# Optimization experiments

Measured on AMD Instinct MI355X. Metric: run time of the kernel, lower is better.

Reference implementation:

```python
import jax, jax.numpy as jnp
import numpy as np

B, T, V, D, P, DEP = 64, 32, 32000, 1024, 8, 4
TAU = 1.0
EPS = 1e-5


def setup_inputs() -> dict:
    key = jax.random.key(0)
    ks = jax.random.split(key, 9)
    s = 0.02
    x = jax.random.randint(ks[0], (B, T), 0, V)
    emb = jax.random.normal(ks[1], (V, D), jnp.float32) * s
    pos = jax.random.normal(ks[2], (T, D), jnp.float32) * s
    # primitive library: n_prims MLPs (Linear -> GELU -> Linear), stacked
    w1 = jax.random.normal(ks[3], (P, D, D), jnp.float32) * s
    b1 = jnp.zeros((P, D), jnp.float32)
    w2 = jax.random.normal(ks[4], (P, D, D), jnp.float32) * s
    b2 = jnp.zeros((P, D), jnp.float32)
    # one selector Linear(dim, n_prims) per depth
    sel_w = jax.random.normal(ks[5], (DEP, P, D), jnp.float32) * s
    sel_b = jnp.zeros((DEP, P), jnp.float32)
    ln_g = jnp.ones((D,), jnp.float32)
    ln_b = jnp.zeros((D,), jnp.float32)
    head_w = jax.random.normal(ks[6], (V, D), jnp.float32) * s
    # fixed gumbel noise (replaces torch's in-op sampling, kept deterministic)
    u = jax.random.uniform(ks[7], (DEP, B, P), jnp.float32, 1e-6, 1.0 - 1e-6)
    gumbel = -jnp.log(-jnp.log(u))
    return dict(x=x, emb=emb, pos=pos, w1=w1, b1=b1, w2=w2, b2=b2,
                sel_w=sel_w, sel_b=sel_b, ln_g=ln_g, ln_b=ln_b,
                head_w=head_w, gumbel=gumbel)


def reference(x, emb, pos, w1, b1, w2, b2, sel_w, sel_b, ln_g, ln_b, head_w, gumbel):
    h = emb[x] + pos[None, :x.shape[1], :]          # [B,T,D]
    div = jnp.float32(0.0)
    unif = jnp.float32(1.0 / P)
    for d in range(DEP):
        ctx = h.mean(axis=1)                         # [B,D]
        logits = ctx @ sel_w[d].T + sel_b[d]         # [B,P]
        weights = jax.nn.softmax((logits + gumbel[d]) / TAU, axis=-1)
        # all primitives over all tokens at once (grouped GEMM), no T loop
        u1 = jax.nn.gelu(jnp.einsum('btd,pde->btpe', h, w1) + b1, approximate=False)
        prim = jnp.einsum('btpe,pef->btpf', u1, w2) + b2   # [B,T,P,D]
        h = h + jnp.einsum('btpf,bp->btf', prim, weights)  # residual add
        avg = weights.mean(axis=0)                   # [P]
        # F.kl_div(avg.log(), uniform, reduction='sum')
        div = div + jnp.sum(unif * (jnp.log(unif) - jnp.log(avg)))
    mu = h.mean(-1, keepdims=True)
    var = ((h - mu) ** 2).mean(-1, keepdims=True)
    hn = (h - mu) * jax.lax.rsqrt(var + EPS) * ln_g + ln_b
    return hn @ head_w.T, div
```

## Files before the change

kernel.cpp:

```cpp
#include <hip/hip_runtime.h>
#include <hip/hip_bf16.h>
#include <math.h>

typedef __bf16 bf16x8 __attribute__((ext_vector_type(8)));
typedef float  f32x4  __attribute__((ext_vector_type(4)));

struct __align__(8) bf16x4s { __hip_bfloat16 a, b, c, d; };

__device__ __forceinline__ void gload_lds16(const void* g, void* l) {
  __builtin_amdgcn_global_load_lds(
      (const __attribute__((address_space(1))) void*)g,
      (__attribute__((address_space(3))) void*)l, 16, 0, 0);
}

__device__ __forceinline__ float fast_gelu(float v) {
  float s = 0.70710678118654752f * v;
  float a = fabsf(s);
  float t = __builtin_amdgcn_rcpf(fmaf(0.3275911f, a, 1.0f));
  float p = t * fmaf(t, fmaf(t, fmaf(t, fmaf(t, 1.061405429f, -1.453152027f),
                                     1.421413741f), -0.284496736f), 0.254829592f);
  float e = __expf(-a * a);
  float er = copysignf(fmaf(-p, e, 1.0f), s);
  return 0.5f * v * (1.0f + er);
}

#define BAR()   asm volatile("s_barrier" ::: "memory")
#define LGKM0() do { asm volatile("s_waitcnt lgkmcnt(0)" ::: "memory"); \
                     __builtin_amdgcn_sched_barrier(0); } while (0)
#define VMC(N)  do { asm volatile("s_waitcnt vmcnt(" #N ")" ::: "memory"); \
                     __builtin_amdgcn_sched_barrier(0); } while (0)
#define P1()    __builtin_amdgcn_s_setprio(1)
#define P0()    __builtin_amdgcn_s_setprio(0)

template<int EPI>
__global__ __launch_bounds__(512, 2)
void gemm_nt(const __hip_bfloat16* __restrict__ A,
             const __hip_bfloat16* __restrict__ B,
             const int K, const int Kc, const int N,
             const float* __restrict__ p0,
             const float* __restrict__ p1,
             float* __restrict__ f32out,
             __hip_bfloat16* __restrict__ bfout)
{
  __shared__ __align__(16) __hip_bfloat16 lds[65536];

  const int tid = threadIdx.x;
  const int lane = tid & 63, wid = tid >> 6;
  const int l15 = lane & 15, l4 = lane >> 4;
  const int r8 = lane >> 3, blk = lane & 7;
  const int wm = wid >> 2, wn = wid & 3;

  const int nx = gridDim.x;
  const int flat = blockIdx.x + nx * blockIdx.y;
  const int q = (nx * gridDim.y) >> 3;
  const int nid = (flat & 7) * q + (flat >> 3);
  const long m0 = (long)(nid % nx) * 256;
  const long n0 = (long)(nid / nx) * 256;

  const int kbeg = blockIdx.z * Kc;
  const int nt = Kc / 64;

  f32x4 acc[8][4] = {};
  bf16x8 ar[4][2], br[4][2];

  auto stageA = [&](int buf, int h, int k0) {
#pragma unroll
    for (int p2 = 0; p2 < 2; ++p2) {
      int ch = p2 * 16 + h * 8 + wid;
      int row = ch * 8 + r8;
      gload_lds16(A + (m0 + row) * (long)K + k0 + ((blk ^ r8) << 3),
                  lds + buf * 16384 + ch * 512);
    }
  };
  auto stageB = [&](int buf, int h, int k0) {
#pragma unroll
    for (int p2 = 0; p2 < 2; ++p2) {
      int ch = (p2 * 2 + (wid >> 2)) * 8 + h * 4 + (wid & 3);
      int row = ch * 8 + r8;
      gload_lds16(B + (n0 + row) * (long)K + k0 + ((blk ^ r8) << 3),
                  lds + 32768 + buf * 16384 + ch * 512);
    }
  };
  auto readA = [&](const __hip_bfloat16* pA, int mih) {
#pragma unroll
    for (int mi = 0; mi < 4; ++mi)
#pragma unroll
      for (int kk = 0; kk < 2; ++kk) {
        int row = wm * 128 + mih * 64 + mi * 16 + l15;
        ar[mi][kk] = *(const bf16x8*)(pA + row * 64 + (((kk * 4 + l4) ^ (row & 7)) << 3));
      }
  };
  auto readB2 = [&](const __hip_bfloat16* pB, int njh) {
#pragma unroll
    for (int nj = 0; nj < 2; ++nj)
#pragma unroll
      for (int kk = 0; kk < 2; ++kk) {
        int row = wn * 64 + njh * 32 + nj * 16 + l15;
        br[njh * 2 + nj][kk] = *(const bf16x8*)(pB + row * 64 + (((kk * 4 + l4) ^ (row & 7)) << 3));
      }
  };
  auto mfma8 = [&](int mib, int njb) {
#pragma unroll
    for (int mi = 0; mi < 4; ++mi)
#pragma unroll
      for (int nj = 0; nj < 2; ++nj)
#pragma unroll
        for (int kk = 0; kk < 2; ++kk)
          acc[mib + mi][njb + nj] = __builtin_amdgcn_mfma_f32_16x16x32_bf16(
              ar[mi][kk], br[njb + nj][kk], acc[mib + mi][njb + nj], 0, 0, 0);
  };

  stageA(0, 0, kbeg);
  stageB(0, 0, kbeg);
  stageB(0, 1, kbeg);
  stageA(0, 1, kbeg);
  stageA(1, 0, kbeg + 64);
  stageB(1, 0, kbeg + 64);
  stageB(1, 1, kbeg + 64);
  VMC(10);
  BAR();

  for (int s = 0; s < nt - 2; ++s) {
    const int b = s & 1;
    const __hip_bfloat16* pA = lds + b * 16384;
    const __hip_bfloat16* pB = lds + 32768 + b * 16384;
    const int k1 = kbeg + (s + 1) * 64, k2 = kbeg + (s + 2) * 64;
    readA(pA, 0); readB2(pB, 0);
    stageA(b ^ 1, 1, k1);
    BAR(); LGKM0();
    P1(); mfma8(0, 0); P0();
    VMC(10); BAR();
    readB2(pB, 1);
    stageA(b, 0, k2);
    BAR(); LGKM0();
    P1(); mfma8(0, 2); P0();
    VMC(10); BAR();
    readA(pA, 1);
    stageB(b, 0, k2);
    BAR(); LGKM0();
    P1(); mfma8(4, 0); P0();
    BAR();
    stageB(b, 1, k2);
    BAR();
    P1(); mfma8(4, 2); P0();
    VMC(10); BAR();
  }

  {
    const int b = (nt - 2) & 1;
    const __hip_bfloat16* pA = lds + b * 16384;
    const __hip_bfloat16* pB = lds + 32768 + b * 16384;
    readA(pA, 0); readB2(pB, 0);
    stageA(b ^ 1, 1, kbeg + (nt - 1) * 64);
    BAR(); LGKM0();
    P1(); mfma8(0, 0); P0();
    VMC(10); BAR();
    readB2(pB, 1);
    BAR(); LGKM0();
    P1(); mfma8(0, 2); P0();
    VMC(8); BAR();
    readA(pA, 1);
    BAR(); LGKM0();
    P1(); mfma8(4, 0); P0();
    BAR();
    BAR();
    P1(); mfma8(4, 2); P0();
    VMC(4); BAR();
  }
  {
    const int b = (nt - 1) & 1;
    const __hip_bfloat16* pA = lds + b * 16384;
    const __hip_bfloat16* pB = lds + 32768 + b * 16384;
    readA(pA, 0); readB2(pB, 0);
    BAR(); LGKM0();
    P1(); mfma8(0, 0); P0();
    VMC(2); BAR();
    readB2(pB, 1);
    BAR(); LGKM0();
    P1(); mfma8(0, 2); P0();
    VMC(0); BAR();
    readA(pA, 1);
    BAR(); LGKM0();
    P1(); mfma8(4, 0); P0();
    BAR();
    BAR();
    P1(); mfma8(4, 2); P0();
    BAR();
  }

  const long slab = (EPI == 2) ? (long)blockIdx.z * (long)(gridDim.x * 256) * N : 0;
#pragma unroll
  for (int mi = 0; mi < 8; ++mi) {
    const long gmb = m0 + wm * 128 + mi * 16 + l4 * 4;
    const int b = (int)(gmb >> 5);
#pragma unroll
    for (int nj = 0; nj < 4; ++nj) {
      const long gn = n0 + wn * 64 + nj * 16 + l15;
      if constexpr (EPI == 0) {
        const int p = (int)(gn >> 10), e = (int)(gn & 1023);
        const float bias = p0[(p << 10) + e];
        const float wpb = p1[(b << 3) + p];
#pragma unroll
        for (int r = 0; r < 4; ++r) {
          float v = fast_gelu(acc[mi][nj][r] + bias) * wpb;
          bfout[(gmb + r) * (long)N + gn] = __float2bfloat16(v);
        }
      } else {
#pragma unroll
        for (int r = 0; r < 4; ++r)
          f32out[slab + (gmb + r) * (long)N + gn] = acc[mi][nj][r];
      }
    }
  }
}

__global__ void cvt_bf16_k(const float* __restrict__ in, __hip_bfloat16* __restrict__ out, long n) {
  long i = ((long)blockIdx.x * blockDim.x + threadIdx.x) * 4;
  if (i >= n) return;
  float4 v = *(const float4*)(in + i);
  *(bf16x4s*)(out + i) = bf16x4s{__float2bfloat16(v.x), __float2bfloat16(v.y),
                                 __float2bfloat16(v.z), __float2bfloat16(v.w)};
}

__global__ void tconv_k(const float* __restrict__ in, __hip_bfloat16* __restrict__ out,
                        long in_bs, long out_rs, long out_bs) {
  __shared__ float tile[32][33];
  int p = blockIdx.z;
  int r0 = blockIdx.y * 32, c0 = blockIdx.x * 32;
  int tx = threadIdx.x, ty = threadIdx.y;
#pragma unroll
  for (int i = 0; i < 32; i += 8)
    tile[ty + i][tx] = in[(long)p * in_bs + (long)(r0 + ty + i) * 1024 + c0 + tx];
  __syncthreads();
#pragma unroll
  for (int i = 0; i < 32; i += 8)
    out[(long)(c0 + ty + i) * out_rs + (long)p * out_bs + (r0 + tx)] =
        __float2bfloat16(tile[tx][ty + i]);
}

__global__ void embed_k(const int* __restrict__ x, const float* __restrict__ emb,
                        const float* __restrict__ pos, float* __restrict__ h,
                        __hip_bfloat16* __restrict__ hb, float* __restrict__ divp) {
  int row = blockIdx.x;
  int t = row & 31;
  int c = threadIdx.x * 4;
  long tok = x[row];
  float4 e = *(const float4*)(emb + tok * 1024 + c);
  float4 q = *(const float4*)(pos + (long)t * 1024 + c);
  float4 v{e.x + q.x, e.y + q.y, e.z + q.z, e.w + q.w};
  *(float4*)(h + (long)row * 1024 + c) = v;
  *(bf16x4s*)(hb + (long)row * 1024 + c) =
      bf16x4s{__float2bfloat16(v.x), __float2bfloat16(v.y),
              __float2bfloat16(v.z), __float2bfloat16(v.w)};
  if (row == 0 && threadIdx.x == 0) *divp = 0.f;
}

__global__ void select_k(const float* __restrict__ h, const float* __restrict__ selw,
                         const float* __restrict__ selb, const float* __restrict__ gum,
                         float* __restrict__ W, int dep) {
  int b = blockIdx.x, tid = threadIdx.x;
  int c = tid * 4;
  float4 s{0.f, 0.f, 0.f, 0.f};
  for (int t = 0; t < 32; ++t) {
    const float4 v = *(const float4*)(h + ((long)(b * 32 + t)) * 1024 + c);
    s.x += v.x; s.y += v.y; s.z += v.z; s.w += v.w;
  }
  float lp[8];
#pragma unroll
  for (int p = 0; p < 8; ++p) {
    const float4 w = *(const float4*)(selw + dep * 8192 + p * 1024 + c);
    lp[p] = (s.x * w.x + s.y * w.y + s.z * w.z + s.w * w.w) * (1.f / 32.f);
  }
  int lane = tid & 63, wid = tid >> 6;
#pragma unroll
  for (int p = 0; p < 8; ++p)
    for (int o = 32; o; o >>= 1) lp[p] += __shfl_down(lp[p], o);
  __shared__ float red[4][8];
  if (lane == 0) {
#pragma unroll
    for (int p = 0; p < 8; ++p) red[wid][p] = lp[p];
  }
  __syncthreads();
  if (tid == 0) {
    float lg[8], mx = -1e30f;
    for (int p = 0; p < 8; ++p) {
      lg[p] = red[0][p] + red[1][p] + red[2][p] + red[3][p]
            + selb[dep * 8 + p] + gum[dep * 512 + b * 8 + p];
      mx = fmaxf(mx, lg[p]);
    }
    float sm = 0.f;
    for (int p = 0; p < 8; ++p) { lg[p] = expf(lg[p] - mx); sm += lg[p]; }
    float inv = 1.f / sm;
    for (int p = 0; p < 8; ++p) W[b * 8 + p] = lg[p] * inv;
  }
}

__global__ void wb2_k(const float* __restrict__ W, const float* __restrict__ b2,
                      float* __restrict__ wb2, float* __restrict__ divp) {
  int b = blockIdx.x;
  int c = threadIdx.x * 4;
  float4 a{0.f, 0.f, 0.f, 0.f};
#pragma unroll
  for (int p = 0; p < 8; ++p) {
    float wp = W[b * 8 + p];
    const float4 v = *(const float4*)(b2 + p * 1024 + c);
    a.x += wp * v.x; a.y += wp * v.y; a.z += wp * v.z; a.w += wp * v.w;
  }
  *(float4*)(wb2 + (long)b * 1024 + c) = a;
  if (b == 0 && threadIdx.x == 0) {
    float s[8] = {0.f, 0.f, 0.f, 0.f, 0.f, 0.f, 0.f, 0.f};
    for (int bb = 0; bb < 64; ++bb)
#pragma unroll
      for (int p = 0; p < 8; ++p) s[p] += W[bb * 8 + p];
    float d = *divp;
    const float u = 0.125f, lu = logf(0.125f);
#pragma unroll
    for (int p = 0; p < 8; ++p) d += u * (lu - logf(s[p] * (1.f / 64.f)));
    *divp = d;
  }
}

__global__ void h_update_k(const float* __restrict__ part, float* __restrict__ h,
                           const float* __restrict__ wb2, __hip_bfloat16* __restrict__ hb) {
  int row = blockIdx.x;
  int c = threadIdx.x * 4;
  long idx = (long)row * 1024 + c;
  float4 a = *(const float4*)(h + idx);
  const float4 w = *(const float4*)(wb2 + (long)(row >> 5) * 1024 + c);
  a.x += w.x; a.y += w.y; a.z += w.z; a.w += w.w;
#pragma unroll
  for (int s = 0; s < 8; ++s) {
    const float4 v = *(const float4*)(part + (long)s * 2097152 + idx);
    a.x += v.x; a.y += v.y; a.z += v.z; a.w += v.w;
  }
  *(float4*)(h + idx) = a;
  *(bf16x4s*)(hb + idx) = bf16x4s{__float2bfloat16(a.x), __float2bfloat16(a.y),
                                  __float2bfloat16(a.z), __float2bfloat16(a.w)};
}

__global__ void ln_k(const float* __restrict__ h, const float* __restrict__ g,
                     const float* __restrict__ be, __hip_bfloat16* __restrict__ hnb,
                     const float* __restrict__ divp, float* __restrict__ divout) {
  int row = blockIdx.x, tid = threadIdx.x;
  int c = tid * 4;
  const float4 v = *(const float4*)(h + (long)row * 1024 + c);
  float s = v.x + v.y + v.z + v.w;
  float q = v.x * v.x + v.y * v.y + v.z * v.z + v.w * v.w;
  for (int o = 32; o; o >>= 1) { s += __shfl_down(s, o); q += __shfl_down(q, o); }
  __shared__ float red[16];
  int lane = tid & 63, wid = tid >> 6;
  if (lane == 0) { red[wid] = s; red[8 + wid] = q; }
  __syncthreads();
  if (tid == 0) {
    float S = red[0] + red[1] + red[2] + red[3];
    float Q = red[8] + red[9] + red[10] + red[11];
    float mu = S * (1.f / 1024.f);
    float var = Q * (1.f / 1024.f) - mu * mu;
    red[0] = mu; red[1] = rsqrtf(var + 1e-5f);
  }
  __syncthreads();
  float mu = red[0], rs = red[1];
  float4 gg = *(const float4*)(g + c), bb = *(const float4*)(be + c);
  *(bf16x4s*)(hnb + (long)row * 1024 + c) =
      bf16x4s{__float2bfloat16((v.x - mu) * rs * gg.x + bb.x),
              __float2bfloat16((v.y - mu) * rs * gg.y + bb.y),
              __float2bfloat16((v.z - mu) * rs * gg.z + bb.z),
              __float2bfloat16((v.w - mu) * rs * gg.w + bb.w)};
  if (row == 0 && tid == 0) *divout = *divp;
}

extern "C" void kernel_launch(void* const* d_in, const int* in_sizes, int n_in,
                              void* d_out, int out_size, void* d_ws, size_t ws_size,
                              hipStream_t stream) {
  (void)in_sizes; (void)n_in; (void)out_size; (void)ws_size;
  const int*   x     = (const int*)  d_in[0];
  const float* emb   = (const float*)d_in[1];
  const float* pos   = (const float*)d_in[2];
  const float* w1    = (const float*)d_in[3];
  const float* b1    = (const float*)d_in[4];
  const float* w2    = (const float*)d_in[5];
  const float* b2    = (const float*)d_in[6];
  const float* selw  = (const float*)d_in[7];
  const float* selb  = (const float*)d_in[8];
  const float* lng   = (const float*)d_in[9];
  const float* lnb   = (const float*)d_in[10];
  const float* headw = (const float*)d_in[11];
  const float* gum   = (const float*)d_in[12];
  float* out = (float*)d_out;

  char* ws = (char*)d_ws;
  __hip_bfloat16* w1t   = (__hip_bfloat16*)(ws);
  __hip_bfloat16* w2t   = (__hip_bfloat16*)(ws + 16777216);
  __hip_bfloat16* headb = (__hip_bfloat16*)(ws + 33554432);
  float*          h     = (float*)(ws + 99090432);
  __hip_bfloat16* hb    = (__hip_bfloat16*)(ws + 107479040);
  __hip_bfloat16* u1    = (__hip_bfloat16*)(ws + 111673344);
  float*          W     = (float*)(ws + 145227776);
  float*          wb2   = (float*)(ws + 145229824);
  float*          divp  = (float*)(ws + 145491968);
  float*          part  = out;

  cvt_bf16_k<<<32000, 256, 0, stream>>>(headw, headb, 32768000L);
  tconv_k<<<dim3(32, 32, 8), dim3(32, 8), 0, stream>>>(w1, w1t, 1L << 20, 1024L, 1L << 20);
  tconv_k<<<dim3(32, 32, 8), dim3(32, 8), 0, stream>>>(w2, w2t, 1L << 20, 8192L, 1024L);
  embed_k<<<2048, 256, 0, stream>>>(x, emb, pos, h, hb, divp);

  for (int d = 0; d < 4; ++d) {
    select_k<<<64, 256, 0, stream>>>(h, selw, selb, gum, W, d);
    wb2_k<<<64, 256, 0, stream>>>(W, b2, wb2, divp);
    gemm_nt<0><<<dim3(8, 32), 512, 0, stream>>>(hb, w1t, 1024, 1024, 8192, b1, W, nullptr, u1);
    gemm_nt<2><<<dim3(8, 4, 8), 512, 0, stream>>>(u1, w2t, 8192, 1024, 1024, nullptr, nullptr, part, nullptr);
    h_update_k<<<2048, 256, 0, stream>>>(part, h, wb2, hb);
  }

  ln_k<<<2048, 256, 0, stream>>>(h, lng, lnb, hb, divp, out + 65536000L);
  gemm_nt<2><<<dim3(8, 125), 512, 0, stream>>>(hb, headb, 1024, 1024, 32000, nullptr, nullptr, out, nullptr);
}
```

Before: 655.8 us.

## Double-buffer GEMM fragment registers and fuse selector with bias-weighting kernel

The GEMM main loop now holds separate early and late register sets for the A and B fragments. It prefetches the next stage's fragments while the MFMAs run on the current ones, which removes the lgkmcnt(0) waits and several barriers per quarter-step. The selector and weighted-bias kernels are merged into one launch, the KL-divergence reduction moves into h_update, and per-depth weights are kept in separate slices. The head GEMM output uses nontemporal stores. The new overlap needs more VGPRs, which could hurt occupancy or cause spills, and the relaxed waits depend on the compiler placing LDS wait counts correctly.

```diff
diff --git a/kernel.cpp b/kernel.cpp
--- a/kernel.cpp
+++ b/kernel.cpp
@@ -25,12 +25,23 @@
 }
 
 #define BAR()   asm volatile("s_barrier" ::: "memory")
-#define LGKM0() do { asm volatile("s_waitcnt lgkmcnt(0)" ::: "memory"); \
-                     __builtin_amdgcn_sched_barrier(0); } while (0)
+#define SB0()   __builtin_amdgcn_sched_barrier(0)
 #define VMC(N)  do { asm volatile("s_waitcnt vmcnt(" #N ")" ::: "memory"); \
                      __builtin_amdgcn_sched_barrier(0); } while (0)
 #define P1()    __builtin_amdgcn_s_setprio(1)
 #define P0()    __builtin_amdgcn_s_setprio(0)
+
+#define MQ(MB, NB, AV, BV)                                                    \
+  do {                                                                        \
+    _Pragma("unroll")                                                         \
+    for (int mi_ = 0; mi_ < 4; ++mi_)                                         \
+      _Pragma("unroll")                                                       \
+      for (int nj_ = 0; nj_ < 2; ++nj_)                                       \
+        _Pragma("unroll")                                                     \
+        for (int kk_ = 0; kk_ < 2; ++kk_)                                     \
+          acc[MB + mi_][NB + nj_] = __builtin_amdgcn_mfma_f32_16x16x32_bf16(  \
+              AV[mi_][kk_], BV[nj_][kk_], acc[MB + mi_][NB + nj_], 0, 0, 0);  \
+  } while (0)
 
 template<int EPI>
 __global__ __launch_bounds__(512, 2)
@@ -61,7 +72,7 @@
   const int nt = Kc / 64;
 
   f32x4 acc[8][4] = {};
-  bf16x8 ar[4][2], br[4][2];
+  bf16x8 arE[4][2], arL[4][2], brE[2][2], brL[2][2];
 
   auto stageA = [&](int buf, int h, int k0) {
 #pragma unroll
@@ -81,33 +92,45 @@
                   lds + 32768 + buf * 16384 + ch * 512);
     }
   };
-  auto readA = [&](const __hip_bfloat16* pA, int mih) {
+  auto readAE = [&](int buf) {
+    const __hip_bfloat16* pA = lds + buf * 16384;
 #pragma unroll
     for (int mi = 0; mi < 4; ++mi)
 #pragma unroll
       for (int kk = 0; kk < 2; ++kk) {
-        int row = wm * 128 + mih * 64 + mi * 16 + l15;
-        ar[mi][kk] = *(const bf16x8*)(pA + row * 64 + (((kk * 4 + l4) ^ (row & 7)) << 3));
+        int row = wm * 128 + mi * 16 + l15;
+        arE[mi][kk] = *(const bf16x8*)(pA + row * 64 + (((kk * 4 + l4) ^ (row & 7)) << 3));
       }
   };
-  auto readB2 = [&](const __hip_bfloat16* pB, int njh) {
+  auto readAL = [&](int buf) {
+    const __hip_bfloat16* pA = lds + buf * 16384;
+#pragma unroll
+    for (int mi = 0; mi < 4; ++mi)
+#pragma unroll
+      for (int kk = 0; kk < 2; ++kk) {
+        int row = wm * 128 + 64 + mi * 16 + l15;
+        arL[mi][kk] = *(const bf16x8*)(pA + row * 64 + (((kk * 4 + l4) ^ (row & 7)) << 3));
+      }
+  };
+  auto readBE = [&](int buf) {
+    const __hip_bfloat16* pB = lds + 32768 + buf * 16384;
 #pragma unroll
     for (int nj = 0; nj < 2; ++nj)
 #pragma unroll
       for (int kk = 0; kk < 2; ++kk) {
-        int row = wn * 64 + njh * 32 + nj * 16 + l15;
-        br[njh * 2 + nj][kk] = *(const bf16x8*)(pB + row * 64 + (((kk * 4 + l4) ^ (row & 7)) << 3));
+        int row = wn * 64 + nj * 16 + l15;
+        brE[nj][kk] = *(const bf16x8*)(pB + row * 64 + (((kk * 4 + l4) ^ (row & 7)) << 3));
       }
   };
-  auto mfma8 = [&](int mib, int njb) {
-#pragma unroll
-    for (int mi = 0; mi < 4; ++mi)
-#pragma unroll
-      for (int nj = 0; nj < 2; ++nj)
-#pragma unroll
-        for (int kk = 0; kk < 2; ++kk)
-          acc[mib + mi][njb + nj] = __builtin_amdgcn_mfma_f32_16x16x32_bf16(
-              ar[mi][kk], br[njb + nj][kk], acc[mib + mi][njb + nj], 0, 0, 0);
+  auto readBL = [&](int buf) {
+    const __hip_bfloat16* pB = lds + 32768 + buf * 16384;
+#pragma unroll
+    for (int nj = 0; nj < 2; ++nj)
+#pragma unroll
+      for (int kk = 0; kk < 2; ++kk) {
+        int row = wn * 64 + 32 + nj * 16 + l15;
+        brL[nj][kk] = *(const bf16x8*)(pB + row * 64 + (((kk * 4 + l4) ^ (row & 7)) << 3));
+      }
   };
 
   stageA(0, 0, kbeg);
@@ -117,75 +140,66 @@
   stageA(1, 0, kbeg + 64);
   stageB(1, 0, kbeg + 64);
   stageB(1, 1, kbeg + 64);
-  VMC(10);
+  VMC(8);
   BAR();
+  readAE(0); readBE(0);
 
   for (int s = 0; s < nt - 2; ++s) {
     const int b = s & 1;
-    const __hip_bfloat16* pA = lds + b * 16384;
-    const __hip_bfloat16* pB = lds + 32768 + b * 16384;
     const int k1 = kbeg + (s + 1) * 64, k2 = kbeg + (s + 2) * 64;
-    readA(pA, 0); readB2(pB, 0);
+    readBL(b);
     stageA(b ^ 1, 1, k1);
-    BAR(); LGKM0();
-    P1(); mfma8(0, 0); P0();
-    VMC(10); BAR();
-    readB2(pB, 1);
+    SB0();
+    P1(); MQ(0, 0, arE, brE); P0();
+    VMC(8); BAR();
+    readAL(b);
     stageA(b, 0, k2);
-    BAR(); LGKM0();
-    P1(); mfma8(0, 2); P0();
-    VMC(10); BAR();
-    readA(pA, 1);
+    SB0();
+    P1(); MQ(0, 2, arE, brL); P0();
+    VMC(8); BAR();
+    readAE(b ^ 1);
     stageB(b, 0, k2);
-    BAR(); LGKM0();
-    P1(); mfma8(4, 0); P0();
-    BAR();
+    SB0();
+    P1(); MQ(4, 0, arL, brE); P0();
+    VMC(8); BAR();
+    readBE(b ^ 1);
     stageB(b, 1, k2);
-    BAR();
-    P1(); mfma8(4, 2); P0();
-    VMC(10); BAR();
+    SB0();
+    P1(); MQ(4, 2, arL, brL); P0();
+    VMC(8); BAR();
   }
 
   {
     const int b = (nt - 2) & 1;
-    const __hip_bfloat16* pA = lds + b * 16384;
-    const __hip_bfloat16* pB = lds + 32768 + b * 16384;
-    readA(pA, 0); readB2(pB, 0);
+    readBL(b);
     stageA(b ^ 1, 1, kbeg + (nt - 1) * 64);
-    BAR(); LGKM0();
-    P1(); mfma8(0, 0); P0();
-    VMC(10); BAR();
-    readB2(pB, 1);
-    BAR(); LGKM0();
-    P1(); mfma8(0, 2); P0();
+    SB0();
+    P1(); MQ(0, 0, arE, brE); P0();
     VMC(8); BAR();
-    readA(pA, 1);
-    BAR(); LGKM0();
-    P1(); mfma8(4, 0); P0();
-    BAR();
-    BAR();
-    P1(); mfma8(4, 2); P0();
+    readAL(b);
+    SB0();
+    P1(); MQ(0, 2, arE, brL); P0();
+    VMC(6); BAR();
+    readAE(b ^ 1);
+    SB0();
+    P1(); MQ(4, 0, arL, brE); P0();
     VMC(4); BAR();
+    readBE(b ^ 1);
+    SB0();
+    P1(); MQ(4, 2, arL, brL); P0();
+    VMC(2); BAR();
   }
   {
     const int b = (nt - 1) & 1;
-    const __hip_bfloat16* pA = lds + b * 16384;
-    const __hip_bfloat16* pB = lds + 32768 + b * 16384;
-    readA(pA, 0); readB2(pB, 0);
-    BAR(); LGKM0();
-    P1(); mfma8(0, 0); P0();
-    VMC(2); BAR();
-    readB2(pB, 1);
-    BAR(); LGKM0();
-    P1(); mfma8(0, 2); P0();
+    readBL(b);
+    SB0();
+    P1(); MQ(0, 0, arE, brE); P0();
     VMC(0); BAR();
-    readA(pA, 1);
-    BAR(); LGKM0();
-    P1(); mfma8(4, 0); P0();
-    BAR();
-    BAR();
-    P1(); mfma8(4, 2); P0();
-    BAR();
+    readAL(b);
+    SB0();
+    P1(); MQ(0, 2, arE, brL); P0();
+    P1(); MQ(4, 0, arL, brE); P0();
+    P1(); MQ(4, 2, arL, brL); P0();
   }
 
   const long slab = (EPI == 2) ? (long)blockIdx.z * (long)(gridDim.x * 256) * N : 0;
@@ -205,10 +219,14 @@
           float v = fast_gelu(acc[mi][nj][r] + bias) * wpb;
           bfout[(gmb + r) * (long)N + gn] = __float2bfloat16(v);
         }
-      } else {
+      } else if constexpr (EPI == 2) {
 #pragma unroll
         for (int r = 0; r < 4; ++r)
           f32out[slab + (gmb + r) * (long)N + gn] = acc[mi][nj][r];
+      } else {
+#pragma unroll
+        for (int r = 0; r < 4; ++r)
+          __builtin_nontemporal_store(acc[mi][nj][r], f32out + (gmb + r) * (long)N + gn);
       }
     }
   }
@@ -255,9 +273,10 @@
   if (row == 0 && threadIdx.x == 0) *divp = 0.f;
 }
 
-__global__ void select_k(const float* __restrict__ h, const float* __restrict__ selw,
-                         const float* __restrict__ selb, const float* __restrict__ gum,
-                         float* __restrict__ W, int dep) {
+__global__ void select_wb2_k(const float* __restrict__ h, const float* __restrict__ selw,
+                             const float* __restrict__ selb, const float* __restrict__ gum,
+                             const float* __restrict__ b2, float* __restrict__ W,
+                             float* __restrict__ wb2, int dep) {
   int b = blockIdx.x, tid = threadIdx.x;
   int c = tid * 4;
   float4 s{0.f, 0.f, 0.f, 0.f};
@@ -276,6 +295,7 @@
   for (int p = 0; p < 8; ++p)
     for (int o = 32; o; o >>= 1) lp[p] += __shfl_down(lp[p], o);
   __shared__ float red[4][8];
+  __shared__ float wsm[8];
   if (lane == 0) {
 #pragma unroll
     for (int p = 0; p < 8; ++p) red[wid][p] = lp[p];
@@ -291,37 +311,22 @@
     float sm = 0.f;
     for (int p = 0; p < 8; ++p) { lg[p] = expf(lg[p] - mx); sm += lg[p]; }
     float inv = 1.f / sm;
-    for (int p = 0; p < 8; ++p) W[b * 8 + p] = lg[p] * inv;
-  }
-}
-
-__global__ void wb2_k(const float* __restrict__ W, const float* __restrict__ b2,
-                      float* __restrict__ wb2, float* __restrict__ divp) {
-  int b = blockIdx.x;
-  int c = threadIdx.x * 4;
+    for (int p = 0; p < 8; ++p) { wsm[p] = lg[p] * inv; W[dep * 512 + b * 8 + p] = lg[p] * inv; }
+  }
+  __syncthreads();
   float4 a{0.f, 0.f, 0.f, 0.f};
 #pragma unroll
   for (int p = 0; p < 8; ++p) {
-    float wp = W[b * 8 + p];
+    float wp = wsm[p];
     const float4 v = *(const float4*)(b2 + p * 1024 + c);
     a.x += wp * v.x; a.y += wp * v.y; a.z += wp * v.z; a.w += wp * v.w;
   }
   *(float4*)(wb2 + (long)b * 1024 + c) = a;
-  if (b == 0 && threadIdx.x == 0) {
-    float s[8] = {0.f, 0.f, 0.f, 0.f, 0.f, 0.f, 0.f, 0.f};
-    for (int bb = 0; bb < 64; ++bb)
-#pragma unroll
-      for (int p = 0; p < 8; ++p) s[p] += W[bb * 8 + p];
-    float d = *divp;
-    const float u = 0.125f, lu = logf(0.125f);
-#pragma unroll
-    for (int p = 0; p < 8; ++p) d += u * (lu - logf(s[p] * (1.f / 64.f)));
-    *divp = d;
-  }
 }
 
 __global__ void h_update_k(const float* __restrict__ part, float* __restrict__ h,
-                           const float* __restrict__ wb2, __hip_bfloat16* __restrict__ hb) {
+                           const float* __restrict__ wb2, __hip_bfloat16* __restrict__ hb,
+                           const float* __restrict__ Wd, float* __restrict__ divp) {
   int row = blockIdx.x;
   int c = threadIdx.x * 4;
   long idx = (long)row * 1024 + c;
@@ -336,6 +341,21 @@
   *(float4*)(h + idx) = a;
   *(bf16x4s*)(hb + idx) = bf16x4s{__float2bfloat16(a.x), __float2bfloat16(a.y),
                                   __float2bfloat16(a.z), __float2bfloat16(a.w)};
+  if (blockIdx.x == 0 && threadIdx.x < 64) {
+    float w8[8];
+#pragma unroll
+    for (int p = 0; p < 8; ++p) w8[p] = Wd[threadIdx.x * 8 + p];
+#pragma unroll
+    for (int p = 0; p < 8; ++p)
+      for (int o = 32; o; o >>= 1) w8[p] += __shfl_down(w8[p], o);
+    if (threadIdx.x == 0) {
+      float d = *divp;
+      const float u = 0.125f, lu = logf(0.125f);
+#pragma unroll
+      for (int p = 0; p < 8; ++p) d += u * (lu - logf(w8[p] * (1.f / 64.f)));
+      *divp = d;
+    }
+  }
 }
 
 __global__ void ln_k(const float* __restrict__ h, const float* __restrict__ g,
@@ -395,9 +415,9 @@
   float*          h     = (float*)(ws + 99090432);
   __hip_bfloat16* hb    = (__hip_bfloat16*)(ws + 107479040);
   __hip_bfloat16* u1    = (__hip_bfloat16*)(ws + 111673344);
-  float*          W     = (float*)(ws + 145227776);
-  float*          wb2   = (float*)(ws + 145229824);
-  float*          divp  = (float*)(ws + 145491968);
+  float*          Wall  = (float*)(ws + 145227776);
+  float*          wb2   = (float*)(ws + 145240064);
+  float*          divp  = (float*)(ws + 145502208);
   float*          part  = out;
 
   cvt_bf16_k<<<32000, 256, 0, stream>>>(headw, headb, 32768000L);
@@ -406,13 +426,12 @@
   embed_k<<<2048, 256, 0, stream>>>(x, emb, pos, h, hb, divp);
 
   for (int d = 0; d < 4; ++d) {
-    select_k<<<64, 256, 0, stream>>>(h, selw, selb, gum, W, d);
-    wb2_k<<<64, 256, 0, stream>>>(W, b2, wb2, divp);
-    gemm_nt<0><<<dim3(8, 32), 512, 0, stream>>>(hb, w1t, 1024, 1024, 8192, b1, W, nullptr, u1);
+    select_wb2_k<<<64, 256, 0, stream>>>(h, selw, selb, gum, b2, Wall, wb2, d);
+    gemm_nt<0><<<dim3(8, 32), 512, 0, stream>>>(hb, w1t, 1024, 1024, 8192, b1, Wall + d * 512, nullptr, u1);
     gemm_nt<2><<<dim3(8, 4, 8), 512, 0, stream>>>(u1, w2t, 8192, 1024, 1024, nullptr, nullptr, part, nullptr);
-    h_update_k<<<2048, 256, 0, stream>>>(part, h, wb2, hb);
+    h_update_k<<<2048, 256, 0, stream>>>(part, h, wb2, hb, Wall + d * 512, divp);
   }
 
   ln_k<<<2048, 256, 0, stream>>>(h, lng, lnb, hb, divp, out + 65536000L);
-  gemm_nt<2><<<dim3(8, 125), 512, 0, stream>>>(hb, headb, 1024, 1024, 32000, nullptr, nullptr, out, nullptr);
-}
+  gemm_nt<3><<<dim3(8, 125), 512, 0, stream>>>(hb, headb, 1024, 1024, 32000, nullptr, nullptr, out, nullptr);
+}
```

Measured after the change: 697.7 us. 6.4% more time.
